# Performance work log

Measured on AMD Instinct MI355X. Metric: run time of the kernel, lower is better.

## Reference

```python
import jax, jax.numpy as jnp
import numpy as np

B, F, D, C, K = 131072, 32, 16, 64, 8  # batch, features, qsvt degree, classes, KAN grid
CLIP = 1.0 - 1e-6


def setup_inputs() -> dict:
    key = jax.random.key(0)
    ks = jax.random.split(key, 7)
    return {
        "X": jax.random.normal(ks[0], (B, F), jnp.float32),
        "qsvt_phases": 0.1 * jax.random.normal(ks[1], (D,), jnp.float32),
        "lcu_weights": jax.random.uniform(ks[2], (F, D), jnp.float32),
        "sum_scale": jnp.ones((F,), jnp.float32) + 0.1 * jax.random.normal(ks[3], (F,), jnp.float32),
        "sum_bias": 0.1 * jax.random.normal(ks[4], (F,), jnp.float32),
        "kan_coeff": jax.random.normal(ks[5], (C, F, K), jnp.float32) / np.sqrt(F * K),
        "kan_bias": jnp.zeros((C,), jnp.float32),
    }


def reference(X, qsvt_phases, lcu_weights, sum_scale, sum_bias, kan_coeff, kan_bias):
    # QSVT: Chebyshev-with-phases polynomial features of each scalar input,
    # vectorized over (batch, feature) instead of the original Python loops.
    degree = qsvt_phases.shape[0]
    grid = kan_coeff.shape[-1]
    theta = jnp.arccos(jnp.clip(X, -CLIP, CLIP))                  # [B,F]
    kd = jnp.arange(1, degree + 1, dtype=X.dtype)                 # [D]
    qsvt_vecs = jnp.cos(theta[..., None] * kd + qsvt_phases)      # [B,F,D]
    # LCU block: normalized linear combination over the degree axis -> scalar per (b,f)
    lcu = jnp.sum(qsvt_vecs * lcu_weights, axis=-1) / (
        jnp.sum(jnp.abs(lcu_weights), axis=-1) + 1e-6)            # [B,F]
    # QuantumSumBlock (one per feature): per-feature affine + tanh squash
    feat = jnp.tanh(sum_scale * lcu + sum_bias)                   # [B,F]
    # KAN layer: Chebyshev basis expansion then per-(class,feature,basis) coefficients
    t2 = jnp.arccos(jnp.clip(feat, -CLIP, CLIP))                  # [B,F]
    kk = jnp.arange(grid, dtype=X.dtype)                          # [K]
    basis = jnp.cos(t2[..., None] * kk)                           # [B,F,K]
    return jnp.einsum('bfk,cfk->bc', basis, kan_coeff) + kan_bias  # [B,C]
```

## Files before the change

### kernel.cpp

```cpp
#include <hip/hip_runtime.h>

#define F 32
#define Dd 16
#define C 64
#define Kk 8
#define CLIPV (1.0f - 1e-6f)
#define CHUNKS 528
#define TABSTRIDE 36
#define NBLK 1024
#define MT 2
#define K2 2.8853900817779268f

typedef short v8s __attribute__((ext_vector_type(8)));
typedef float v4f __attribute__((ext_vector_type(4)));
typedef float v2f __attribute__((ext_vector_type(2)));

static __device__ inline unsigned cvtpk(float lo, float hi) {
    unsigned r;
    asm("v_cvt_pk_bf16_f32 %0, %1, %2" : "=v"(r) : "v"(lo), "v"(hi));
    return r;
}

__global__ __launch_bounds__(256, 4) void qkan_kernel(
    const float* __restrict__ X,
    const float* __restrict__ phases,
    const float* __restrict__ lcu_w,
    const float* __restrict__ sscale,
    const float* __restrict__ sbias,
    const float* __restrict__ coeff,
    const float* __restrict__ kbias,
    float* __restrict__ out)
{
    __shared__ unsigned short s_basis[F * CHUNKS];
    __shared__ float s_tab[F * TABSTRIDE];

    const int tid = threadIdx.x;
    const int lane = tid & 63;
    const int wu = __builtin_amdgcn_readfirstlane(tid >> 6);
    const int h = lane >> 4;
    const int r16 = lane & 15;

    const int rb0 = blockIdx.x * (MT * 64);
    const float* xr0 = X + (size_t)(rb0 + lane) * F + wu * 8;
    const float4 xa0 = *reinterpret_cast<const float4*>(xr0);
    const float4 xb0 = *reinterpret_cast<const float4*>(xr0 + 4);
    const float* xr1 = xr0 + 64 * F;
    const float4 xa1 = *reinterpret_cast<const float4*>(xr1);
    const float4 xb1 = *reinterpret_cast<const float4*>(xr1 + 4);

    for (int idx = tid; idx < F * Dd; idx += 256) {
        const int f = idx >> 4, d = idx & 15;
        float asum = 0.f;
#pragma unroll
        for (int dd = 0; dd < Dd; ++dd) asum += fabsf(lcu_w[f * Dd + dd]);
        const float sc = K2 * sscale[f] / (asum + 1e-6f);
        float sp, cp;
        __sincosf(phases[d], &sp, &cp);
        const float wv = lcu_w[f * Dd + d];
        s_tab[f * TABSTRIDE + 2 * d]     = sc * wv * cp;
        s_tab[f * TABSTRIDE + 2 * d + 1] = -sc * wv * sp;
        if (d == 0) s_tab[f * TABSTRIDE + 32] = K2 * sbias[f];
    }

    v8s Bfr[8];
    const int cidx = wu * 16 + r16;
#pragma unroll
    for (int q = 0; q < 8; ++q) {
        const int f = 4 * q + h;
        const float* gp = coeff + ((size_t)(cidx * F + f) * Kk);
        const float4 g0 = *reinterpret_cast<const float4*>(gp);
        const float4 g1 = *reinterpret_cast<const float4*>(gp + 4);
        union { unsigned u[4]; v8s v; } bb;
        bb.u[0] = cvtpk(g0.x, g0.y);
        bb.u[1] = cvtpk(g0.z, g0.w);
        bb.u[2] = cvtpk(g1.x, g1.y);
        bb.u[3] = cvtpk(g1.z, g1.w);
        Bfr[q] = bb.v;
    }
    const float biasreg = kbias[cidx];

    __syncthreads();

    for (int mt = 0; mt < MT; ++mt) {
        const int row_base = rb0 + mt * 64;
        if (mt) __syncthreads();

        {
            const float4 xa = mt ? xa1 : xa0;
            const float4 xb = mt ? xb1 : xb0;
            const float xv[8] = {xa.x, xa.y, xa.z, xa.w, xb.x, xb.y, xb.z, xb.w};
#pragma unroll
            for (int fl = 0; fl < 8; ++fl) {
                const int f = wu * 8 + fl;
                const float* tfp = s_tab + f * TABSTRIDE;
                const v2f* tf2 = reinterpret_cast<const v2f*>(tfp);
                const float fb = tfp[32];
                const float x = fminf(fmaxf(xv[fl], -CLIPV), CLIPV);
                const float s1 = sqrtf(fmaxf(__builtin_fmaf(-x, x, 1.f), 0.f));
                const float tx = x + x;
                const v2f tx2 = {tx, tx};
                v2f w = {0.f, 0.f}, wp = {0.f, 0.f};
#pragma unroll
                for (int j = 15; j >= 0; --j) {
                    const v2f wn = (tf2[j] - wp) + tx2 * w;
                    wp = w;
                    w = wn;
                }
                float z = fb - wp.x;
                z = __builtin_fmaf(x, w.x, z);
                z = __builtin_fmaf(s1, w.y, z);
                float e;
                asm("v_exp_f32 %0, %1" : "=v"(e) : "v"(z));
                const float rr = __builtin_amdgcn_rcpf(e + 1.f);
                const float t = __builtin_fmaf(-2.f, rr, 1.f);
                const float t2 = t + t;
                const float b1 = t;
                const float b2 = t2 * b1 - 1.f;
                const float b3 = t2 * b2 - b1;
                const float b4 = t2 * b3 - b2;
                const float b5 = t2 * b4 - b3;
                const float b6 = t2 * b5 - b4;
                const float b7 = t2 * b6 - b5;
                uint4 pk;
                pk.x = cvtpk(1.f, b1);
                pk.y = cvtpk(b2, b3);
                pk.z = cvtpk(b4, b5);
                pk.w = cvtpk(b6, b7);
                *reinterpret_cast<uint4*>(&s_basis[f * CHUNKS + lane * 8]) = pk;
            }
        }
        __syncthreads();

        {
#pragma unroll
            for (int t = 0; t < 4; ++t) {
                v4f acc = {0.f, 0.f, 0.f, 0.f};
#pragma unroll
                for (int q = 0; q < 8; ++q) {
                    const v8s a = *reinterpret_cast<const v8s*>(
                        &s_basis[(4 * q + h) * CHUNKS + (t * 16 + r16) * 8]);
                    acc = __builtin_amdgcn_mfma_f32_16x16x32_bf16(a, Bfr[q], acc, 0, 0, 0);
                }
                const int row0 = row_base + t * 16 + h * 4;
#pragma unroll
                for (int i = 0; i < 4; ++i) {
                    out[(size_t)(row0 + i) * C + cidx] = acc[i] + biasreg;
                }
            }
        }
    }
}

extern "C" void kernel_launch(void* const* d_in, const int* in_sizes, int n_in,
                              void* d_out, int out_size, void* d_ws, size_t ws_size,
                              hipStream_t stream) {
    const float* X  = (const float*)d_in[0];
    const float* ph = (const float*)d_in[1];
    const float* lw = (const float*)d_in[2];
    const float* ss = (const float*)d_in[3];
    const float* sb = (const float*)d_in[4];
    const float* kc = (const float*)d_in[5];
    const float* kb = (const float*)d_in[6];
    float* out = (float*)d_out;
    qkan_kernel<<<dim3(NBLK), dim3(256), 0, stream>>>(X, ph, lw, ss, sb, kc, kb, out);
}
```

Before: 29.43 us.

## Compute basis directly in MFMA A-fragment layout per wave, dropping LDS staging

Each wave now owns 64 rows and computes the Chebyshev basis for the exact (row, feature) slots its MFMA A-operand needs, so it feeds the MFMA from registers instead of writing to and reading back from a shared basis buffer. Each wave keeps all four column tiles of the KAN coefficients in registers (32 fragments) and software-prefetches the next 16 rows of X. This removes the LDS basis buffer and the mid-loop block barriers, but raises register pressure (launch bounds cut to 2 blocks/CU) and halves the grid to 512 blocks, which may reduce latency hiding.

```diff
diff --git a/kernel.cpp b/kernel.cpp
--- a/kernel.cpp
+++ b/kernel.cpp
@@ -5,11 +5,9 @@
 #define C 64
 #define Kk 8
 #define CLIPV (1.0f - 1e-6f)
-#define CHUNKS 528
 #define TABSTRIDE 36
-#define NBLK 1024
-#define MT 2
 #define K2 2.8853900817779268f
+#define NBLK 512
 
 typedef short v8s __attribute__((ext_vector_type(8)));
 typedef float v4f __attribute__((ext_vector_type(4)));
@@ -21,7 +19,7 @@
     return r;
 }
 
-__global__ __launch_bounds__(256, 4) void qkan_kernel(
+__global__ __launch_bounds__(256, 2) void qkan_kernel(
     const float* __restrict__ X,
     const float* __restrict__ phases,
     const float* __restrict__ lcu_w,
@@ -31,7 +29,6 @@
     const float* __restrict__ kbias,
     float* __restrict__ out)
 {
-    __shared__ unsigned short s_basis[F * CHUNKS];
     __shared__ float s_tab[F * TABSTRIDE];
 
     const int tid = threadIdx.x;
@@ -40,13 +37,35 @@
     const int h = lane >> 4;
     const int r16 = lane & 15;
 
-    const int rb0 = blockIdx.x * (MT * 64);
-    const float* xr0 = X + (size_t)(rb0 + lane) * F + wu * 8;
-    const float4 xa0 = *reinterpret_cast<const float4*>(xr0);
-    const float4 xb0 = *reinterpret_cast<const float4*>(xr0 + 4);
-    const float* xr1 = xr0 + 64 * F;
-    const float4 xa1 = *reinterpret_cast<const float4*>(xr1);
-    const float4 xb1 = *reinterpret_cast<const float4*>(xr1 + 4);
+    const int row00 = (blockIdx.x * 4 + wu) * 64;
+
+    float xq[8];
+    {
+        const float* xp = X + (size_t)(row00 + r16) * F + h;
+#pragma unroll
+        for (int m = 0; m < 8; ++m) xq[m] = xp[4 * m];
+    }
+
+    v8s Bfr[8][4];
+#pragma unroll
+    for (int q = 0; q < 8; ++q) {
+#pragma unroll
+        for (int nt = 0; nt < 4; ++nt) {
+            const float* gp = coeff + ((size_t)((nt * 16 + r16) * F + 4 * q + h) * Kk);
+            const float4 g0 = *reinterpret_cast<const float4*>(gp);
+            const float4 g1 = *reinterpret_cast<const float4*>(gp + 4);
+            union { unsigned u[4]; v8s v; } bb;
+            bb.u[0] = cvtpk(g0.x, g0.y);
+            bb.u[1] = cvtpk(g0.z, g0.w);
+            bb.u[2] = cvtpk(g1.x, g1.y);
+            bb.u[3] = cvtpk(g1.z, g1.w);
+            Bfr[q][nt] = bb.v;
+        }
+    }
+    const float bias0 = kbias[r16];
+    const float bias1 = kbias[16 + r16];
+    const float bias2 = kbias[32 + r16];
+    const float bias3 = kbias[48 + r16];
 
     for (int idx = tid; idx < F * Dd; idx += 256) {
         const int f = idx >> 4, d = idx & 15;
@@ -61,92 +80,80 @@
         s_tab[f * TABSTRIDE + 2 * d + 1] = -sc * wv * sp;
         if (d == 0) s_tab[f * TABSTRIDE + 32] = K2 * sbias[f];
     }
-
-    v8s Bfr[8];
-    const int cidx = wu * 16 + r16;
-#pragma unroll
-    for (int q = 0; q < 8; ++q) {
-        const int f = 4 * q + h;
-        const float* gp = coeff + ((size_t)(cidx * F + f) * Kk);
-        const float4 g0 = *reinterpret_cast<const float4*>(gp);
-        const float4 g1 = *reinterpret_cast<const float4*>(gp + 4);
-        union { unsigned u[4]; v8s v; } bb;
-        bb.u[0] = cvtpk(g0.x, g0.y);
-        bb.u[1] = cvtpk(g0.z, g0.w);
-        bb.u[2] = cvtpk(g1.x, g1.y);
-        bb.u[3] = cvtpk(g1.z, g1.w);
-        Bfr[q] = bb.v;
-    }
-    const float biasreg = kbias[cidx];
-
     __syncthreads();
 
-    for (int mt = 0; mt < MT; ++mt) {
-        const int row_base = rb0 + mt * 64;
-        if (mt) __syncthreads();
+#pragma unroll
+    for (int it = 0; it < 4; ++it) {
+        const int row0 = row00 + it * 16;
 
-        {
-            const float4 xa = mt ? xa1 : xa0;
-            const float4 xb = mt ? xb1 : xb0;
-            const float xv[8] = {xa.x, xa.y, xa.z, xa.w, xb.x, xb.y, xb.z, xb.w};
+        float xn[8];
+        if (it < 3) {
+            const float* xp = X + (size_t)(row0 + 16 + r16) * F + h;
 #pragma unroll
-            for (int fl = 0; fl < 8; ++fl) {
-                const int f = wu * 8 + fl;
-                const float* tfp = s_tab + f * TABSTRIDE;
-                const v2f* tf2 = reinterpret_cast<const v2f*>(tfp);
-                const float fb = tfp[32];
-                const float x = fminf(fmaxf(xv[fl], -CLIPV), CLIPV);
-                const float s1 = sqrtf(fmaxf(__builtin_fmaf(-x, x, 1.f), 0.f));
-                const float tx = x + x;
-                const v2f tx2 = {tx, tx};
-                v2f w = {0.f, 0.f}, wp = {0.f, 0.f};
+            for (int m = 0; m < 8; ++m) xn[m] = xp[4 * m];
+        }
+
+        v4f acc0 = {0.f, 0.f, 0.f, 0.f};
+        v4f acc1 = {0.f, 0.f, 0.f, 0.f};
+        v4f acc2 = {0.f, 0.f, 0.f, 0.f};
+        v4f acc3 = {0.f, 0.f, 0.f, 0.f};
+
 #pragma unroll
-                for (int j = 15; j >= 0; --j) {
-                    const v2f wn = (tf2[j] - wp) + tx2 * w;
-                    wp = w;
-                    w = wn;
-                }
-                float z = fb - wp.x;
-                z = __builtin_fmaf(x, w.x, z);
-                z = __builtin_fmaf(s1, w.y, z);
-                float e;
-                asm("v_exp_f32 %0, %1" : "=v"(e) : "v"(z));
-                const float rr = __builtin_amdgcn_rcpf(e + 1.f);
-                const float t = __builtin_fmaf(-2.f, rr, 1.f);
-                const float t2 = t + t;
-                const float b1 = t;
-                const float b2 = t2 * b1 - 1.f;
-                const float b3 = t2 * b2 - b1;
-                const float b4 = t2 * b3 - b2;
-                const float b5 = t2 * b4 - b3;
-                const float b6 = t2 * b5 - b4;
-                const float b7 = t2 * b6 - b5;
-                uint4 pk;
-                pk.x = cvtpk(1.f, b1);
-                pk.y = cvtpk(b2, b3);
-                pk.z = cvtpk(b4, b5);
-                pk.w = cvtpk(b6, b7);
-                *reinterpret_cast<uint4*>(&s_basis[f * CHUNKS + lane * 8]) = pk;
+        for (int q = 0; q < 8; ++q) {
+            const int f = 4 * q + h;
+            const float* tfp = s_tab + f * TABSTRIDE;
+            const v2f* tf2 = reinterpret_cast<const v2f*>(tfp);
+            const float fb = tfp[32];
+            const float x = fminf(fmaxf(xq[q], -CLIPV), CLIPV);
+            const float s1 = sqrtf(fmaxf(__builtin_fmaf(-x, x, 1.f), 0.f));
+            const float tx = x + x;
+            const v2f tx2 = {tx, tx};
+            v2f w = {0.f, 0.f}, wp = {0.f, 0.f};
+#pragma unroll
+            for (int j = 15; j >= 0; --j) {
+                const v2f wn = (tf2[j] - wp) + tx2 * w;
+                wp = w;
+                w = wn;
             }
+            float z = fb - wp.x;
+            z = __builtin_fmaf(x, w.x, z);
+            z = __builtin_fmaf(s1, w.y, z);
+            float e;
+            asm("v_exp_f32 %0, %1" : "=v"(e) : "v"(z));
+            const float rr = __builtin_amdgcn_rcpf(e + 1.f);
+            const float t = __builtin_fmaf(-2.f, rr, 1.f);
+            const float t2 = t + t;
+            const float b1 = t;
+            const float b2 = t2 * b1 - 1.f;
+            const float b3 = t2 * b2 - b1;
+            const float b4 = t2 * b3 - b2;
+            const float b5 = t2 * b4 - b3;
+            const float b6 = t2 * b5 - b4;
+            const float b7 = t2 * b6 - b5;
+            union { unsigned u[4]; v8s v; } pa;
+            pa.u[0] = cvtpk(1.f, b1);
+            pa.u[1] = cvtpk(b2, b3);
+            pa.u[2] = cvtpk(b4, b5);
+            pa.u[3] = cvtpk(b6, b7);
+            acc0 = __builtin_amdgcn_mfma_f32_16x16x32_bf16(pa.v, Bfr[q][0], acc0, 0, 0, 0);
+            acc1 = __builtin_amdgcn_mfma_f32_16x16x32_bf16(pa.v, Bfr[q][1], acc1, 0, 0, 0);
+            acc2 = __builtin_amdgcn_mfma_f32_16x16x32_bf16(pa.v, Bfr[q][2], acc2, 0, 0, 0);
+            acc3 = __builtin_amdgcn_mfma_f32_16x16x32_bf16(pa.v, Bfr[q][3], acc3, 0, 0, 0);
         }
-        __syncthreads();
 
-        {
+        const int orow = row0 + h * 4;
 #pragma unroll
-            for (int t = 0; t < 4; ++t) {
-                v4f acc = {0.f, 0.f, 0.f, 0.f};
+        for (int i = 0; i < 4; ++i) {
+            float* op = out + (size_t)(orow + i) * C + r16;
+            op[0]  = acc0[i] + bias0;
+            op[16] = acc1[i] + bias1;
+            op[32] = acc2[i] + bias2;
+            op[48] = acc3[i] + bias3;
+        }
+
+        if (it < 3) {
 #pragma unroll
-                for (int q = 0; q < 8; ++q) {
-                    const v8s a = *reinterpret_cast<const v8s*>(
-                        &s_basis[(4 * q + h) * CHUNKS + (t * 16 + r16) * 8]);
-                    acc = __builtin_amdgcn_mfma_f32_16x16x32_bf16(a, Bfr[q], acc, 0, 0, 0);
-                }
-                const int row0 = row_base + t * 16 + h * 4;
-#pragma unroll
-                for (int i = 0; i < 4; ++i) {
-                    out[(size_t)(row0 + i) * C + cidx] = acc[i] + biasreg;
-                }
-            }
+            for (int m = 0; m < 8; ++m) xq[m] = xn[m];
         }
     }
 }
```

Result: slower. 42.65 us (+44.9%).

## Map threads to one feature each and keep Clenshaw coefficients in registers

Applied to the files above, without the earlier changes.

Each thread now owns a single feature and eight rows, so its per-feature LCU coefficients (16 cos/sin pairs plus bias) are computed once into registers rather than read from a shared-memory table. This removes the table and its initial barrier. X for the second tile is prefetched during the first tile's compute, and the basis LDS stride changes to 536. The cost is higher register pressure from 32 coefficient registers plus prefetch buffers, and X loads become strided scalar loads (32 lanes across contiguous features) instead of float4 loads.

```diff
diff --git a/kernel.cpp b/kernel.cpp
--- a/kernel.cpp
+++ b/kernel.cpp
@@ -5,11 +5,10 @@
 #define C 64
 #define Kk 8
 #define CLIPV (1.0f - 1e-6f)
-#define CHUNKS 528
-#define TABSTRIDE 36
+#define CHUNKU 536
+#define K2 2.8853900817779268f
 #define NBLK 1024
 #define MT 2
-#define K2 2.8853900817779268f
 
 typedef short v8s __attribute__((ext_vector_type(8)));
 typedef float v4f __attribute__((ext_vector_type(4)));
@@ -31,43 +30,52 @@
     const float* __restrict__ kbias,
     float* __restrict__ out)
 {
-    __shared__ unsigned short s_basis[F * CHUNKS];
-    __shared__ float s_tab[F * TABSTRIDE];
+    __shared__ unsigned short s_basis[F * CHUNKU];
 
     const int tid = threadIdx.x;
     const int lane = tid & 63;
     const int wu = __builtin_amdgcn_readfirstlane(tid >> 6);
     const int h = lane >> 4;
     const int r16 = lane & 15;
+    const int fe = tid & 31;
+    const int rg = tid >> 5;
 
     const int rb0 = blockIdx.x * (MT * 64);
-    const float* xr0 = X + (size_t)(rb0 + lane) * F + wu * 8;
-    const float4 xa0 = *reinterpret_cast<const float4*>(xr0);
-    const float4 xb0 = *reinterpret_cast<const float4*>(xr0 + 4);
-    const float* xr1 = xr0 + 64 * F;
-    const float4 xa1 = *reinterpret_cast<const float4*>(xr1);
-    const float4 xb1 = *reinterpret_cast<const float4*>(xr1 + 4);
 
-    for (int idx = tid; idx < F * Dd; idx += 256) {
-        const int f = idx >> 4, d = idx & 15;
+    float xq[8];
+    {
+        const float* xp = X + (size_t)(rb0 + rg * 8) * F + fe;
+#pragma unroll
+        for (int m = 0; m < 8; ++m) xq[m] = xp[m * F];
+    }
+
+    v2f cc[16];
+    float fbias;
+    {
+        const float* lwf = lcu_w + fe * Dd;
+        float wv[16];
         float asum = 0.f;
 #pragma unroll
-        for (int dd = 0; dd < Dd; ++dd) asum += fabsf(lcu_w[f * Dd + dd]);
-        const float sc = K2 * sscale[f] / (asum + 1e-6f);
-        float sp, cp;
-        __sincosf(phases[d], &sp, &cp);
-        const float wv = lcu_w[f * Dd + d];
-        s_tab[f * TABSTRIDE + 2 * d]     = sc * wv * cp;
-        s_tab[f * TABSTRIDE + 2 * d + 1] = -sc * wv * sp;
-        if (d == 0) s_tab[f * TABSTRIDE + 32] = K2 * sbias[f];
+        for (int d = 0; d < Dd; ++d) {
+            wv[d] = lwf[d];
+            asum += fabsf(wv[d]);
+        }
+        const float sc = K2 * sscale[fe] / (asum + 1e-6f);
+#pragma unroll
+        for (int d = 0; d < Dd; ++d) {
+            float sp, cp;
+            __sincosf(phases[d], &sp, &cp);
+            cc[d][0] = sc * wv[d] * cp;
+            cc[d][1] = -sc * wv[d] * sp;
+        }
+        fbias = K2 * sbias[fe];
     }
 
     v8s Bfr[8];
     const int cidx = wu * 16 + r16;
 #pragma unroll
     for (int q = 0; q < 8; ++q) {
-        const int f = 4 * q + h;
-        const float* gp = coeff + ((size_t)(cidx * F + f) * Kk);
+        const float* gp = coeff + ((size_t)(cidx * F + 4 * q + h) * Kk);
         const float4 g0 = *reinterpret_cast<const float4*>(gp);
         const float4 g1 = *reinterpret_cast<const float4*>(gp + 4);
         union { unsigned u[4]; v8s v; } bb;
@@ -79,74 +87,74 @@
     }
     const float biasreg = kbias[cidx];
 
-    __syncthreads();
-
     for (int mt = 0; mt < MT; ++mt) {
         const int row_base = rb0 + mt * 64;
         if (mt) __syncthreads();
 
-        {
-            const float4 xa = mt ? xa1 : xa0;
-            const float4 xb = mt ? xb1 : xb0;
-            const float xv[8] = {xa.x, xa.y, xa.z, xa.w, xb.x, xb.y, xb.z, xb.w};
+        float xn[8];
+        if (mt + 1 < MT) {
+            const float* xp = X + (size_t)(row_base + 64 + rg * 8) * F + fe;
 #pragma unroll
-            for (int fl = 0; fl < 8; ++fl) {
-                const int f = wu * 8 + fl;
-                const float* tfp = s_tab + f * TABSTRIDE;
-                const v2f* tf2 = reinterpret_cast<const v2f*>(tfp);
-                const float fb = tfp[32];
-                const float x = fminf(fmaxf(xv[fl], -CLIPV), CLIPV);
-                const float s1 = sqrtf(fmaxf(__builtin_fmaf(-x, x, 1.f), 0.f));
-                const float tx = x + x;
-                const v2f tx2 = {tx, tx};
-                v2f w = {0.f, 0.f}, wp = {0.f, 0.f};
+            for (int m = 0; m < 8; ++m) xn[m] = xp[m * F];
+        }
+
 #pragma unroll
-                for (int j = 15; j >= 0; --j) {
-                    const v2f wn = (tf2[j] - wp) + tx2 * w;
-                    wp = w;
-                    w = wn;
-                }
-                float z = fb - wp.x;
-                z = __builtin_fmaf(x, w.x, z);
-                z = __builtin_fmaf(s1, w.y, z);
-                float e;
-                asm("v_exp_f32 %0, %1" : "=v"(e) : "v"(z));
-                const float rr = __builtin_amdgcn_rcpf(e + 1.f);
-                const float t = __builtin_fmaf(-2.f, rr, 1.f);
-                const float t2 = t + t;
-                const float b1 = t;
-                const float b2 = t2 * b1 - 1.f;
-                const float b3 = t2 * b2 - b1;
-                const float b4 = t2 * b3 - b2;
-                const float b5 = t2 * b4 - b3;
-                const float b6 = t2 * b5 - b4;
-                const float b7 = t2 * b6 - b5;
-                uint4 pk;
-                pk.x = cvtpk(1.f, b1);
-                pk.y = cvtpk(b2, b3);
-                pk.z = cvtpk(b4, b5);
-                pk.w = cvtpk(b6, b7);
-                *reinterpret_cast<uint4*>(&s_basis[f * CHUNKS + lane * 8]) = pk;
+        for (int m = 0; m < 8; ++m) {
+            const int row = rg * 8 + m;
+            const float x = fminf(fmaxf(xq[m], -CLIPV), CLIPV);
+            const float s1 = sqrtf(fmaxf(__builtin_fmaf(-x, x, 1.f), 0.f));
+            const float tx = x + x;
+            const v2f tx2 = {tx, tx};
+            v2f w = {0.f, 0.f}, wp = {0.f, 0.f};
+#pragma unroll
+            for (int j = 15; j >= 0; --j) {
+                const v2f wn = (cc[j] - wp) + tx2 * w;
+                wp = w;
+                w = wn;
             }
+            float z = fbias - wp[0];
+            z = __builtin_fmaf(x, w[0], z);
+            z = __builtin_fmaf(s1, w[1], z);
+            float e;
+            asm("v_exp_f32 %0, %1" : "=v"(e) : "v"(z));
+            const float rr = __builtin_amdgcn_rcpf(e + 1.f);
+            const float t = __builtin_fmaf(-2.f, rr, 1.f);
+            const float t2 = t + t;
+            const float b1 = t;
+            const float b2 = t2 * b1 - 1.f;
+            const float b3 = t2 * b2 - b1;
+            const float b4 = t2 * b3 - b2;
+            const float b5 = t2 * b4 - b3;
+            const float b6 = t2 * b5 - b4;
+            const float b7 = t2 * b6 - b5;
+            uint4 pk;
+            pk.x = cvtpk(1.f, b1);
+            pk.y = cvtpk(b2, b3);
+            pk.z = cvtpk(b4, b5);
+            pk.w = cvtpk(b6, b7);
+            *reinterpret_cast<uint4*>(&s_basis[fe * CHUNKU + row * 8]) = pk;
         }
         __syncthreads();
 
-        {
 #pragma unroll
-            for (int t = 0; t < 4; ++t) {
-                v4f acc = {0.f, 0.f, 0.f, 0.f};
+        for (int t = 0; t < 4; ++t) {
+            v4f acc = {0.f, 0.f, 0.f, 0.f};
 #pragma unroll
-                for (int q = 0; q < 8; ++q) {
-                    const v8s a = *reinterpret_cast<const v8s*>(
-                        &s_basis[(4 * q + h) * CHUNKS + (t * 16 + r16) * 8]);
-                    acc = __builtin_amdgcn_mfma_f32_16x16x32_bf16(a, Bfr[q], acc, 0, 0, 0);
-                }
-                const int row0 = row_base + t * 16 + h * 4;
+            for (int q = 0; q < 8; ++q) {
+                const v8s a = *reinterpret_cast<const v8s*>(
+                    &s_basis[(4 * q + h) * CHUNKU + (t * 16 + r16) * 8]);
+                acc = __builtin_amdgcn_mfma_f32_16x16x32_bf16(a, Bfr[q], acc, 0, 0, 0);
+            }
+            const int row0 = row_base + t * 16 + h * 4;
 #pragma unroll
-                for (int i = 0; i < 4; ++i) {
-                    out[(size_t)(row0 + i) * C + cidx] = acc[i] + biasreg;
-                }
+            for (int i = 0; i < 4; ++i) {
+                out[(size_t)(row0 + i) * C + cidx] = acc[i] + biasreg;
             }
+        }
+
+        if (mt + 1 < MT) {
+#pragma unroll
+            for (int m = 0; m < 8; ++m) xq[m] = xn[m];
         }
     }
 }
```

Measured after the change: 27.59 us. -6.3%, faster.

## Split table prep into separate kernel and restructure main kernel to 512-thread 64-row blocks

Applied to the files above, without the earlier changes.

Moves the per-feature LCU/phase table computation into a tiny prep kernel that writes a global table, so the main kernel no longer recomputes it per block. The main kernel now uses 512 threads per block over 64 rows (2048 blocks), stages X through a transposed, XOR-swizzled shared buffer with coalesced loads, and spreads the feature and MFMA work across 8 waves. Barriers only wait on LDS counters. This adds a second kernel launch and global-memory reads of the table in the hot loop.

```diff
diff --git a/kernel.cpp b/kernel.cpp
--- a/kernel.cpp
+++ b/kernel.cpp
@@ -5,15 +5,15 @@
 #define C 64
 #define Kk 8
 #define CLIPV (1.0f - 1e-6f)
-#define CHUNKS 528
 #define TABSTRIDE 36
-#define NBLK 1024
-#define MT 2
 #define K2 2.8853900817779268f
+#define NBLK 2048
 
 typedef short v8s __attribute__((ext_vector_type(8)));
 typedef float v4f __attribute__((ext_vector_type(4)));
 typedef float v2f __attribute__((ext_vector_type(2)));
+
+__device__ float g_tab[F * TABSTRIDE];
 
 static __device__ inline unsigned cvtpk(float lo, float hi) {
     unsigned r;
@@ -21,18 +21,38 @@
     return r;
 }
 
-__global__ __launch_bounds__(256, 4) void qkan_kernel(
+#define BAR_LGKM() do {                                          \
+    asm volatile("s_waitcnt lgkmcnt(0)" ::: "memory");           \
+    __builtin_amdgcn_s_barrier();                                \
+    asm volatile("" ::: "memory");                               \
+} while (0)
+
+__global__ void qkan_prep(const float* __restrict__ phases,
+                          const float* __restrict__ lcu_w,
+                          const float* __restrict__ sscale,
+                          const float* __restrict__ sbias) {
+    const int idx = threadIdx.x;
+    const int f = idx >> 4, d = idx & 15;
+    float asum = 0.f;
+#pragma unroll
+    for (int dd = 0; dd < Dd; ++dd) asum += fabsf(lcu_w[f * Dd + dd]);
+    const float sc = K2 * sscale[f] / (asum + 1e-6f);
+    float sp, cp;
+    __sincosf(phases[d], &sp, &cp);
+    const float wv = lcu_w[f * Dd + d];
+    g_tab[f * TABSTRIDE + 2 * d]     = sc * wv * cp;
+    g_tab[f * TABSTRIDE + 2 * d + 1] = -sc * wv * sp;
+    if (d == 0) g_tab[f * TABSTRIDE + 32] = K2 * sbias[f];
+}
+
+__global__ __launch_bounds__(512, 8) void qkan_kernel(
     const float* __restrict__ X,
-    const float* __restrict__ phases,
-    const float* __restrict__ lcu_w,
-    const float* __restrict__ sscale,
-    const float* __restrict__ sbias,
     const float* __restrict__ coeff,
     const float* __restrict__ kbias,
     float* __restrict__ out)
 {
-    __shared__ unsigned short s_basis[F * CHUNKS];
-    __shared__ float s_tab[F * TABSTRIDE];
+    __shared__ float s_xT[F * 64];
+    __shared__ unsigned short s_basis[F * 512];
 
     const int tid = threadIdx.x;
     const int lane = tid & 63;
@@ -40,34 +60,69 @@
     const int h = lane >> 4;
     const int r16 = lane & 15;
 
-    const int rb0 = blockIdx.x * (MT * 64);
-    const float* xr0 = X + (size_t)(rb0 + lane) * F + wu * 8;
-    const float4 xa0 = *reinterpret_cast<const float4*>(xr0);
-    const float4 xb0 = *reinterpret_cast<const float4*>(xr0 + 4);
-    const float* xr1 = xr0 + 64 * F;
-    const float4 xa1 = *reinterpret_cast<const float4*>(xr1);
-    const float4 xb1 = *reinterpret_cast<const float4*>(xr1 + 4);
+    const int rb = blockIdx.x * 64;
 
-    for (int idx = tid; idx < F * Dd; idx += 256) {
-        const int f = idx >> 4, d = idx & 15;
-        float asum = 0.f;
+    {
+        const float* xp = X + (size_t)rb * F;
 #pragma unroll
-        for (int dd = 0; dd < Dd; ++dd) asum += fabsf(lcu_w[f * Dd + dd]);
-        const float sc = K2 * sscale[f] / (asum + 1e-6f);
-        float sp, cp;
-        __sincosf(phases[d], &sp, &cp);
-        const float wv = lcu_w[f * Dd + d];
-        s_tab[f * TABSTRIDE + 2 * d]     = sc * wv * cp;
-        s_tab[f * TABSTRIDE + 2 * d + 1] = -sc * wv * sp;
-        if (d == 0) s_tab[f * TABSTRIDE + 32] = K2 * sbias[f];
+        for (int k = 0; k < 4; ++k) {
+            const int idx = tid + k * 512;
+            const int f = idx & 31;
+            const int lr = idx >> 5;
+            s_xT[f * 64 + (lr ^ f)] = xp[idx];
+        }
     }
+    BAR_LGKM();
 
+#pragma unroll
+    for (int p = 0; p < 4; ++p) {
+        const int fu = __builtin_amdgcn_readfirstlane(p * 8 + wu);
+        const float* tfp = g_tab + fu * TABSTRIDE;
+        const v2f* tf2 = reinterpret_cast<const v2f*>(tfp);
+        const float fb = tfp[32];
+        const float x0 = s_xT[fu * 64 + (lane ^ fu)];
+        const float x = fminf(fmaxf(x0, -CLIPV), CLIPV);
+        const float s1 = sqrtf(fmaxf(__builtin_fmaf(-x, x, 1.f), 0.f));
+        const float tx = x + x;
+        const v2f tx2 = {tx, tx};
+        v2f w = {0.f, 0.f}, wp = {0.f, 0.f};
+#pragma unroll
+        for (int j = 15; j >= 0; --j) {
+            const v2f wn = (tf2[j] - wp) + tx2 * w;
+            wp = w;
+            w = wn;
+        }
+        float z = fb - wp[0];
+        z = __builtin_fmaf(x, w[0], z);
+        z = __builtin_fmaf(s1, w[1], z);
+        float e;
+        asm("v_exp_f32 %0, %1" : "=v"(e) : "v"(z));
+        const float rr = __builtin_amdgcn_rcpf(e + 1.f);
+        const float t = __builtin_fmaf(-2.f, rr, 1.f);
+        const float t2 = t + t;
+        const float b1 = t;
+        const float b2 = t2 * b1 - 1.f;
+        const float b3 = t2 * b2 - b1;
+        const float b4 = t2 * b3 - b2;
+        const float b5 = t2 * b4 - b3;
+        const float b6 = t2 * b5 - b4;
+        const float b7 = t2 * b6 - b5;
+        uint4 pk;
+        pk.x = cvtpk(1.f, b1);
+        pk.y = cvtpk(b2, b3);
+        pk.z = cvtpk(b4, b5);
+        pk.w = cvtpk(b6, b7);
+        *reinterpret_cast<uint4*>(&s_basis[fu * 512 + lane * 8]) = pk;
+    }
+    BAR_LGKM();
+
+    const int ct = wu & 3;
+    const int rt0 = (wu >> 2) * 2;
+    const int cidx = ct * 16 + r16;
     v8s Bfr[8];
-    const int cidx = wu * 16 + r16;
 #pragma unroll
     for (int q = 0; q < 8; ++q) {
-        const int f = 4 * q + h;
-        const float* gp = coeff + ((size_t)(cidx * F + f) * Kk);
+        const float* gp = coeff + ((size_t)(cidx * F + 4 * q + h) * Kk);
         const float4 g0 = *reinterpret_cast<const float4*>(gp);
         const float4 g1 = *reinterpret_cast<const float4*>(gp + 4);
         union { unsigned u[4]; v8s v; } bb;
@@ -79,74 +134,20 @@
     }
     const float biasreg = kbias[cidx];
 
-    __syncthreads();
-
-    for (int mt = 0; mt < MT; ++mt) {
-        const int row_base = rb0 + mt * 64;
-        if (mt) __syncthreads();
-
-        {
-            const float4 xa = mt ? xa1 : xa0;
-            const float4 xb = mt ? xb1 : xb0;
-            const float xv[8] = {xa.x, xa.y, xa.z, xa.w, xb.x, xb.y, xb.z, xb.w};
 #pragma unroll
-            for (int fl = 0; fl < 8; ++fl) {
-                const int f = wu * 8 + fl;
-                const float* tfp = s_tab + f * TABSTRIDE;
-                const v2f* tf2 = reinterpret_cast<const v2f*>(tfp);
-                const float fb = tfp[32];
-                const float x = fminf(fmaxf(xv[fl], -CLIPV), CLIPV);
-                const float s1 = sqrtf(fmaxf(__builtin_fmaf(-x, x, 1.f), 0.f));
-                const float tx = x + x;
-                const v2f tx2 = {tx, tx};
-                v2f w = {0.f, 0.f}, wp = {0.f, 0.f};
+    for (int j = 0; j < 2; ++j) {
+        const int rt = rt0 + j;
+        v4f acc = {0.f, 0.f, 0.f, 0.f};
 #pragma unroll
-                for (int j = 15; j >= 0; --j) {
-                    const v2f wn = (tf2[j] - wp) + tx2 * w;
-                    wp = w;
-                    w = wn;
-                }
-                float z = fb - wp.x;
-                z = __builtin_fmaf(x, w.x, z);
-                z = __builtin_fmaf(s1, w.y, z);
-                float e;
-                asm("v_exp_f32 %0, %1" : "=v"(e) : "v"(z));
-                const float rr = __builtin_amdgcn_rcpf(e + 1.f);
-                const float t = __builtin_fmaf(-2.f, rr, 1.f);
-                const float t2 = t + t;
-                const float b1 = t;
-                const float b2 = t2 * b1 - 1.f;
-                const float b3 = t2 * b2 - b1;
-                const float b4 = t2 * b3 - b2;
-                const float b5 = t2 * b4 - b3;
-                const float b6 = t2 * b5 - b4;
-                const float b7 = t2 * b6 - b5;
-                uint4 pk;
-                pk.x = cvtpk(1.f, b1);
-                pk.y = cvtpk(b2, b3);
-                pk.z = cvtpk(b4, b5);
-                pk.w = cvtpk(b6, b7);
-                *reinterpret_cast<uint4*>(&s_basis[f * CHUNKS + lane * 8]) = pk;
-            }
+        for (int q = 0; q < 8; ++q) {
+            const v8s a = *reinterpret_cast<const v8s*>(
+                &s_basis[(4 * q + h) * 512 + (rt * 16 + r16) * 8]);
+            acc = __builtin_amdgcn_mfma_f32_16x16x32_bf16(a, Bfr[q], acc, 0, 0, 0);
         }
-        __syncthreads();
-
-        {
+        const int row0 = rb + rt * 16 + h * 4;
 #pragma unroll
-            for (int t = 0; t < 4; ++t) {
-                v4f acc = {0.f, 0.f, 0.f, 0.f};
-#pragma unroll
-                for (int q = 0; q < 8; ++q) {
-                    const v8s a = *reinterpret_cast<const v8s*>(
-                        &s_basis[(4 * q + h) * CHUNKS + (t * 16 + r16) * 8]);
-                    acc = __builtin_amdgcn_mfma_f32_16x16x32_bf16(a, Bfr[q], acc, 0, 0, 0);
-                }
-                const int row0 = row_base + t * 16 + h * 4;
-#pragma unroll
-                for (int i = 0; i < 4; ++i) {
-                    out[(size_t)(row0 + i) * C + cidx] = acc[i] + biasreg;
-                }
-            }
+        for (int i = 0; i < 4; ++i) {
+            out[(size_t)(row0 + i) * C + cidx] = acc[i] + biasreg;
         }
     }
 }
@@ -162,5 +163,7 @@
     const float* kc = (const float*)d_in[5];
     const float* kb = (const float*)d_in[6];
     float* out = (float*)d_out;
-    qkan_kernel<<<dim3(NBLK), dim3(256), 0, stream>>>(X, ph, lw, ss, sb, kc, kb, out);
+
+    qkan_prep<<<dim3(1), dim3(512), 0, stream>>>(ph, lw, ss, sb);
+    qkan_kernel<<<dim3(NBLK), dim3(512), 0, stream>>>(X, kc, kb, out);
 }
```

Result: slower. 63.46 us (+115.6%).
